# Kernel optimization log

Hardware: AMD Instinct MI355X
Metric: run time of the kernel (lower is better)

## Reference

```python
import jax, jax.numpy as jnp
import numpy as np
from jax.ops import segment_sum


def gcn_conv(x, src, dst, W, b, num_nodes):
    # PyG GCNConv: x' = D^{-1/2} (A + I) D^{-1/2} (x @ W) + b
    loops = jnp.arange(num_nodes, dtype=src.dtype)
    s = jnp.concatenate([src, loops])  # source of each edge (incl. self-loops)
    d = jnp.concatenate([dst, loops])  # destination of each edge
    ones = jnp.ones(s.shape[0], dtype=x.dtype)
    deg = segment_sum(ones, d, num_segments=num_nodes)  # in-degree incl. self-loop
    dinv = jnp.where(deg > 0, jax.lax.rsqrt(deg), 0.0)
    norm = dinv[s] * dinv[d]  # [E+N]
    h = x @ W  # [N, C_out] dense transform first (C_out <= C_in typical)
    msg = h[s] * norm[:, None]  # gather + scale  [E+N, C_out]
    out = segment_sum(msg, d, num_segments=num_nodes)  # scatter-add
    return out + b


def setup_inputs() -> dict:
    key = jax.random.key(0)
    k1, k2, k3, k4 = jax.random.split(key, 4)
    N, E = 100000, 1600000
    C_in, C_out = 64, 32
    C_hid = 2 * C_out
    x = jax.random.normal(k1, (N, C_in), dtype=jnp.float32)
    edge_index = jax.random.randint(k2, (2, E), 0, N, dtype=jnp.int64)
    # Glorot-style init for the linear weights, zero bias (PyG defaults)
    W1 = jax.random.normal(k3, (C_in, C_hid), dtype=jnp.float32) * (1.0 / np.sqrt(C_in))
    b1 = jnp.zeros((C_hid,), dtype=jnp.float32)
    W2 = jax.random.normal(k4, (C_hid, C_out), dtype=jnp.float32) * (1.0 / np.sqrt(C_hid))
    b2 = jnp.zeros((C_out,), dtype=jnp.float32)
    return {"x": x, "edge_index": edge_index, "num_nodes": N,
            "W1": W1, "b1": b1, "W2": W2, "b2": b2}


def reference(x, edge_index, num_nodes, W1, b1, W2, b2):
    src, dst = edge_index[0], edge_index[1]
    h = gcn_conv(x, src, dst, W1, b1, num_nodes)
    h = jax.nn.relu(h)
    out = gcn_conv(h, src, dst, W2, b2, num_nodes)
    return out
```

## Files before the change

kernel.cpp:

```cpp
#include <hip/hip_runtime.h>


constexpr int CAP = 8192;
constexpr int NBMAX = 512;

__device__ inline unsigned short f2bf(float f) {
    unsigned u = __float_as_uint(f);
    u += 0x7fff + ((u >> 16) & 1);
    return (unsigned short)(u >> 16);
}
__device__ inline float bflo(unsigned u) { return __uint_as_float(u << 16); }
__device__ inline float bfhi(unsigned u) { return __uint_as_float(u & 0xffff0000u); }

__global__ __launch_bounds__(256) void p1_bin(const int* __restrict__ src,
                                              const int* __restrict__ dst,
                                              int* __restrict__ bucketCursor,
                                              unsigned* __restrict__ staging, int E, int NB) {
    __shared__ int cnt[NBMAX];
    __shared__ int cur[NBMAX];
    int tid = threadIdx.x;
    for (int i = tid; i < NB; i += 256) cnt[i] = 0;
    __syncthreads();
    int e0 = blockIdx.x * 4096;
#pragma unroll
    for (int k = 0; k < 16; ++k) {
        int e = e0 + k * 256 + tid;
        if (e < E) atomicAdd(&cnt[dst[e] >> 8], 1);
    }
    __syncthreads();
    for (int i = tid; i < NB; i += 256) {
        int c = cnt[i];
        cur[i] = c ? atomicAdd(&bucketCursor[i], c) : 0;
    }
    __syncthreads();
#pragma unroll
    for (int k = 0; k < 16; ++k) {
        int e = e0 + k * 256 + tid;
        if (e < E) {
            int d = dst[e];
            int b = d >> 8;
            int slot = atomicAdd(&cur[b], 1);
            staging[(size_t)b * CAP + slot] = ((unsigned)src[e] << 8) | (unsigned)(d & 255);
        }
    }
}

__global__ __launch_bounds__(512) void scan_buckets(const int* __restrict__ bucketCursor,
                                                    int* __restrict__ bucketBase,
                                                    int* __restrict__ rp, int NB, int N, int E) {
    __shared__ int s[NBMAX];
    int tid = threadIdx.x;
    int v = (tid < NB) ? bucketCursor[tid] : 0;
    s[tid] = v;
    __syncthreads();
    for (int off = 1; off < 512; off <<= 1) {
        int t = (tid >= off) ? s[tid - off] : 0;
        __syncthreads();
        s[tid] += t;
        __syncthreads();
    }
    if (tid < NB) bucketBase[tid] = s[tid] - v;
    if (tid == 0) {
        bucketBase[NB] = E;
        rp[N] = E;
    }
}

__global__ __launch_bounds__(256) void p2_csr(const unsigned* __restrict__ staging,
                                              const int* __restrict__ bucketBase,
                                              int* __restrict__ rp, int* __restrict__ col,
                                              float* __restrict__ dinv, int N) {
    __shared__ int deg[256];
    __shared__ int scn[256];
    __shared__ int cur[256];
    int b = blockIdx.x;
    int tid = threadIdx.x;
    int base = bucketBase[b];
    int size = bucketBase[b + 1] - base;
    const unsigned* st = staging + (size_t)b * CAP;
    deg[tid] = 0;
    __syncthreads();
    for (int i = tid; i < size; i += 256) atomicAdd(&deg[st[i] & 255u], 1);
    __syncthreads();
    int g = b * 256 + tid;
    int d = deg[tid];
    if (g < N) dinv[g] = rsqrtf((float)(d + 1));
    scn[tid] = d;
    __syncthreads();
    for (int off = 1; off < 256; off <<= 1) {
        int t = (tid >= off) ? scn[tid - off] : 0;
        __syncthreads();
        scn[tid] += t;
        __syncthreads();
    }
    int excl = scn[tid] - d;
    if (g < N) rp[g] = base + excl;
    cur[tid] = excl;
    __syncthreads();
    for (int i = tid; i < size; i += 256) {
        unsigned pk = st[i];
        int pos = atomicAdd(&cur[pk & 255u], 1);
        col[base + pos] = (int)(pk >> 8);
    }
}

__global__ __launch_bounds__(256) void gemm1(const float* __restrict__ X,
                                             const float* __restrict__ W,
                                             const float* __restrict__ dinv,
                                             unsigned short* __restrict__ Hout, int N) {
    constexpr int XS = 65;
    __shared__ float Xs[128 * XS];
    __shared__ float Ws[64 * 64];
    int tid = threadIdx.x;
    int rowBase = blockIdx.x * 128;
    const float4* Wv = (const float4*)W;
    float4* Wsv = (float4*)Ws;
    for (int i = tid; i < 64 * 64 / 4; i += 256) Wsv[i] = Wv[i];
    const float4* Xv = (const float4*)X;
    for (int v = tid; v < 128 * 16; v += 256) {
        int r = v >> 4, j = v & 15;
        int gr = rowBase + r;
        float4 t = make_float4(0.f, 0.f, 0.f, 0.f);
        if (gr < N) t = Xv[(size_t)gr * 16 + j];
        int b = r * XS + j * 4;
        Xs[b] = t.x;
        Xs[b + 1] = t.y;
        Xs[b + 2] = t.z;
        Xs[b + 3] = t.w;
    }
    __syncthreads();
    int cg = tid % 8, rg = tid / 8;
    int c0 = cg * 8, r0 = rg * 4;
    float acc[4][8];
#pragma unroll
    for (int i = 0; i < 4; ++i)
#pragma unroll
        for (int j = 0; j < 8; ++j) acc[i][j] = 0.f;
#pragma unroll 8
    for (int k = 0; k < 64; ++k) {
        float4 w0 = *(const float4*)&Ws[k * 64 + c0];
        float4 w1 = *(const float4*)&Ws[k * 64 + c0 + 4];
        float xr[4];
#pragma unroll
        for (int i = 0; i < 4; ++i) xr[i] = Xs[(r0 + i) * XS + k];
#pragma unroll
        for (int i = 0; i < 4; ++i) {
            acc[i][0] = fmaf(xr[i], w0.x, acc[i][0]);
            acc[i][1] = fmaf(xr[i], w0.y, acc[i][1]);
            acc[i][2] = fmaf(xr[i], w0.z, acc[i][2]);
            acc[i][3] = fmaf(xr[i], w0.w, acc[i][3]);
            acc[i][4] = fmaf(xr[i], w1.x, acc[i][4]);
            acc[i][5] = fmaf(xr[i], w1.y, acc[i][5]);
            acc[i][6] = fmaf(xr[i], w1.z, acc[i][6]);
            acc[i][7] = fmaf(xr[i], w1.w, acc[i][7]);
        }
    }
#pragma unroll
    for (int i = 0; i < 4; ++i) {
        int row = rowBase + r0 + i;
        if (row >= N) continue;
        float dn = dinv[row];
        unsigned pk[4];
#pragma unroll
        for (int j = 0; j < 4; ++j) {
            unsigned lo = f2bf(acc[i][2 * j] * dn);
            unsigned hi = f2bf(acc[i][2 * j + 1] * dn);
            pk[j] = lo | (hi << 16);
        }
        *(uint4*)(Hout + (size_t)row * 64 + c0) = make_uint4(pk[0], pk[1], pk[2], pk[3]);
    }
}

__global__ __launch_bounds__(256) void agg1_gemm2(
    const uint4* __restrict__ hs1, const float* __restrict__ dinv, const int* __restrict__ rp,
    const int* __restrict__ col, const float* __restrict__ b1, const float* __restrict__ W2,
    unsigned short* __restrict__ h2, int N) {
    constexpr int RS = 68;
    __shared__ float rows[32 * RS];
    __shared__ float Ws2[64 * 32];
    int tid = threadIdx.x;
    const float4* W2v = (const float4*)W2;
    float4* Ws2v = (float4*)Ws2;
    for (int i = tid; i < 64 * 32 / 4; i += 256) Ws2v[i] = W2v[i];

    int r = tid >> 3, q = tid & 7;
    int node = blockIdx.x * 32 + r;
    float acc[8];
#pragma unroll
    for (int j = 0; j < 8; ++j) acc[j] = 0.f;
    float dn = 0.f;
    if (node < N) {
        dn = dinv[node];
        uint4 u = hs1[(size_t)node * 8 + q];
        acc[0] = bflo(u.x); acc[1] = bfhi(u.x);
        acc[2] = bflo(u.y); acc[3] = bfhi(u.y);
        acc[4] = bflo(u.z); acc[5] = bfhi(u.z);
        acc[6] = bflo(u.w); acc[7] = bfhi(u.w);
        int e0 = rp[node], e1 = rp[node + 1];
        int e = e0;
#define ACC8(U)                               \
    acc[0] += bflo(U.x); acc[1] += bfhi(U.x); \
    acc[2] += bflo(U.y); acc[3] += bfhi(U.y); \
    acc[4] += bflo(U.z); acc[5] += bfhi(U.z); \
    acc[6] += bflo(U.w); acc[7] += bfhi(U.w);
        for (; e + 4 <= e1; e += 4) {
            int s0 = col[e], s1 = col[e + 1], s2 = col[e + 2], s3 = col[e + 3];
            uint4 u0 = hs1[(size_t)s0 * 8 + q];
            uint4 u1 = hs1[(size_t)s1 * 8 + q];
            uint4 u2 = hs1[(size_t)s2 * 8 + q];
            uint4 u3 = hs1[(size_t)s3 * 8 + q];
            ACC8(u0) ACC8(u1) ACC8(u2) ACC8(u3)
        }
        for (; e < e1; ++e) {
            uint4 uu = hs1[(size_t)col[e] * 8 + q];
            ACC8(uu)
        }
#undef ACC8
        const float4* bv = (const float4*)b1;
        float4 bb0 = bv[q * 2], bb1 = bv[q * 2 + 1];
        acc[0] = fmaxf(fmaf(acc[0], dn, bb0.x), 0.f);
        acc[1] = fmaxf(fmaf(acc[1], dn, bb0.y), 0.f);
        acc[2] = fmaxf(fmaf(acc[2], dn, bb0.z), 0.f);
        acc[3] = fmaxf(fmaf(acc[3], dn, bb0.w), 0.f);
        acc[4] = fmaxf(fmaf(acc[4], dn, bb1.x), 0.f);
        acc[5] = fmaxf(fmaf(acc[5], dn, bb1.y), 0.f);
        acc[6] = fmaxf(fmaf(acc[6], dn, bb1.z), 0.f);
        acc[7] = fmaxf(fmaf(acc[7], dn, bb1.w), 0.f);
    }
    float* myrow = &rows[r * RS + q * 8];
    *(float4*)myrow = make_float4(acc[0], acc[1], acc[2], acc[3]);
    *(float4*)(myrow + 4) = make_float4(acc[4], acc[5], acc[6], acc[7]);
    __syncthreads();

    if (node >= N) return;
    int c0 = q * 4;
    float acc2[4] = {0.f, 0.f, 0.f, 0.f};
    const float* row = &rows[r * RS];
#pragma unroll
    for (int k4 = 0; k4 < 16; ++k4) {
        float4 xq = *(const float4*)&row[k4 * 4];
        float4 wa = *(const float4*)&Ws2[(k4 * 4 + 0) * 32 + c0];
        float4 wb = *(const float4*)&Ws2[(k4 * 4 + 1) * 32 + c0];
        float4 wc = *(const float4*)&Ws2[(k4 * 4 + 2) * 32 + c0];
        float4 wd = *(const float4*)&Ws2[(k4 * 4 + 3) * 32 + c0];
        acc2[0] = fmaf(xq.x, wa.x, acc2[0]);
        acc2[1] = fmaf(xq.x, wa.y, acc2[1]);
        acc2[2] = fmaf(xq.x, wa.z, acc2[2]);
        acc2[3] = fmaf(xq.x, wa.w, acc2[3]);
        acc2[0] = fmaf(xq.y, wb.x, acc2[0]);
        acc2[1] = fmaf(xq.y, wb.y, acc2[1]);
        acc2[2] = fmaf(xq.y, wb.z, acc2[2]);
        acc2[3] = fmaf(xq.y, wb.w, acc2[3]);
        acc2[0] = fmaf(xq.z, wc.x, acc2[0]);
        acc2[1] = fmaf(xq.z, wc.y, acc2[1]);
        acc2[2] = fmaf(xq.z, wc.z, acc2[2]);
        acc2[3] = fmaf(xq.z, wc.w, acc2[3]);
        acc2[0] = fmaf(xq.w, wd.x, acc2[0]);
        acc2[1] = fmaf(xq.w, wd.y, acc2[1]);
        acc2[2] = fmaf(xq.w, wd.z, acc2[2]);
        acc2[3] = fmaf(xq.w, wd.w, acc2[3]);
    }
    unsigned p0 = f2bf(acc2[0] * dn) | ((unsigned)f2bf(acc2[1] * dn) << 16);
    unsigned p1 = f2bf(acc2[2] * dn) | ((unsigned)f2bf(acc2[3] * dn) << 16);
    *(uint2*)(h2 + (size_t)node * 32 + c0) = make_uint2(p0, p1);
}

__global__ __launch_bounds__(256) void agg2(const uint4* __restrict__ hs2,
                                            const float* __restrict__ dinv,
                                            const int* __restrict__ rp,
                                            const int* __restrict__ col,
                                            const float* __restrict__ bias,
                                            float* __restrict__ out, int N) {
    int t = blockIdx.x * blockDim.x + threadIdx.x;
    int node = t >> 2, q = t & 3;
    if (node >= N) return;
    float acc[8];
    uint4 u = hs2[(size_t)node * 4 + q];
    acc[0] = bflo(u.x); acc[1] = bfhi(u.x);
    acc[2] = bflo(u.y); acc[3] = bfhi(u.y);
    acc[4] = bflo(u.z); acc[5] = bfhi(u.z);
    acc[6] = bflo(u.w); acc[7] = bfhi(u.w);
    int e0 = rp[node], e1 = rp[node + 1];
    int e = e0;
#define ACC8(U)                               \
    acc[0] += bflo(U.x); acc[1] += bfhi(U.x); \
    acc[2] += bflo(U.y); acc[3] += bfhi(U.y); \
    acc[4] += bflo(U.z); acc[5] += bfhi(U.z); \
    acc[6] += bflo(U.w); acc[7] += bfhi(U.w);
    for (; e + 4 <= e1; e += 4) {
        int s0 = col[e], s1 = col[e + 1], s2 = col[e + 2], s3 = col[e + 3];
        uint4 u0 = hs2[(size_t)s0 * 4 + q];
        uint4 u1 = hs2[(size_t)s1 * 4 + q];
        uint4 u2 = hs2[(size_t)s2 * 4 + q];
        uint4 u3 = hs2[(size_t)s3 * 4 + q];
        ACC8(u0) ACC8(u1) ACC8(u2) ACC8(u3)
    }
    for (; e < e1; ++e) {
        uint4 uu = hs2[(size_t)col[e] * 4 + q];
        ACC8(uu)
    }
#undef ACC8
    float dn = dinv[node];
    const float4* bv = (const float4*)bias;
    float4 b0 = bv[q * 2], b1 = bv[q * 2 + 1];
    float4 r0, r1;
    r0.x = fmaf(acc[0], dn, b0.x);
    r0.y = fmaf(acc[1], dn, b0.y);
    r0.z = fmaf(acc[2], dn, b0.z);
    r0.w = fmaf(acc[3], dn, b0.w);
    r1.x = fmaf(acc[4], dn, b1.x);
    r1.y = fmaf(acc[5], dn, b1.y);
    r1.z = fmaf(acc[6], dn, b1.z);
    r1.w = fmaf(acc[7], dn, b1.w);
    float4* ov = (float4*)(out + (size_t)node * 32 + q * 8);
    ov[0] = r0;
    ov[1] = r1;
}

extern "C" void kernel_launch(void* const* d_in, const int* in_sizes, int n_in,
                              void* d_out, int out_size, void* d_ws, size_t ws_size,
                              hipStream_t stream) {
    const float* x = (const float*)d_in[0];
    const int* ei = (const int*)d_in[1];
    const float* W1 = (const float*)d_in[3];
    const float* b1 = (const float*)d_in[4];
    const float* W2 = (const float*)d_in[5];
    const float* b2 = (const float*)d_in[6];

    constexpr int CIN = 64, CHID = 64;
    const int N = in_sizes[0] / CIN;
    const int E = in_sizes[1] / 2;
    const int* src = ei;
    const int* dst = ei + E;
    const int NB = (N + 255) >> 8;

    char* p = (char*)d_ws;
    auto carve = [&](size_t bytes) -> void* {
        void* q = (void*)p;
        p += (bytes + 255) & ~(size_t)255;
        return q;
    };
    int* bucketCursor = (int*)carve((size_t)NB * 4);
    int* bucketBase = (int*)carve((size_t)(NB + 1) * 4);
    int* rp = (int*)carve((size_t)(N + 1) * 4);
    int* col = (int*)carve((size_t)E * 4);
    float* dinv = (float*)carve((size_t)N * 4);
    unsigned* staging = (unsigned*)carve((size_t)NB * CAP * 4);
    unsigned short* h1 = (unsigned short*)carve((size_t)N * CHID * 2);
    unsigned short* h2 = (unsigned short*)staging;

    hipMemsetAsync(bucketCursor, 0, (size_t)NB * 4, stream);
    p1_bin<<<(E + 4095) / 4096, 256, 0, stream>>>(src, dst, bucketCursor, staging, E, NB);
    scan_buckets<<<1, 512, 0, stream>>>(bucketCursor, bucketBase, rp, NB, N, E);
    p2_csr<<<NB, 256, 0, stream>>>(staging, bucketBase, rp, col, dinv, N);

    gemm1<<<(N + 127) / 128, 256, 0, stream>>>(x, W1, dinv, h1, N);
    agg1_gemm2<<<(N + 31) / 32, 256, 0, stream>>>((const uint4*)h1, dinv, rp, col, b1, W2, h2, N);
    agg2<<<((size_t)N * 4 + 255) / 256, 256, 0, stream>>>((const uint4*)h2, dinv, rp, col, b2,
                                                          (float*)d_out, N);
}
```

Measured before the change: 207.6 us.

## Fold bucket scan into CSR build and add dynamic node scheduling to aggregations

Removes the single-block scan_buckets launch: each p2_csr block now redundantly prefix-sums the bucket counts in shared memory to find its own base. Both aggregation kernels now handle more nodes per block (64 and 128), and node groups take the next node from a shared-memory atomic counter. This balances uneven per-node degree inside a block. The second GEMM is remapped to four threads per node with eight outputs each and uint4 stores. The cost is extra redundant scan work per block and atomic traffic in shared memory.

```diff
diff --git a/kernel.cpp b/kernel.cpp
--- a/kernel.cpp
+++ b/kernel.cpp
@@ -45,41 +45,33 @@
     }
 }
 
-__global__ __launch_bounds__(512) void scan_buckets(const int* __restrict__ bucketCursor,
-                                                    int* __restrict__ bucketBase,
-                                                    int* __restrict__ rp, int NB, int N, int E) {
-    __shared__ int s[NBMAX];
-    int tid = threadIdx.x;
-    int v = (tid < NB) ? bucketCursor[tid] : 0;
-    s[tid] = v;
-    __syncthreads();
-    for (int off = 1; off < 512; off <<= 1) {
-        int t = (tid >= off) ? s[tid - off] : 0;
-        __syncthreads();
-        s[tid] += t;
-        __syncthreads();
-    }
-    if (tid < NB) bucketBase[tid] = s[tid] - v;
-    if (tid == 0) {
-        bucketBase[NB] = E;
-        rp[N] = E;
-    }
-}
-
 __global__ __launch_bounds__(256) void p2_csr(const unsigned* __restrict__ staging,
-                                              const int* __restrict__ bucketBase,
+                                              const int* __restrict__ bucketCursor,
                                               int* __restrict__ rp, int* __restrict__ col,
-                                              float* __restrict__ dinv, int N) {
+                                              float* __restrict__ dinv, int N, int E, int NB) {
+    __shared__ int sb[NBMAX];
     __shared__ int deg[256];
     __shared__ int scn[256];
     __shared__ int cur[256];
     int b = blockIdx.x;
     int tid = threadIdx.x;
-    int base = bucketBase[b];
-    int size = bucketBase[b + 1] - base;
+    int i1 = tid, i2 = tid + 256;
+    sb[i1] = (i1 < NB) ? bucketCursor[i1] : 0;
+    sb[i2] = (i2 < NB) ? bucketCursor[i2] : 0;
+    deg[tid] = 0;
+    __syncthreads();
+    for (int off = 1; off < NBMAX; off <<= 1) {
+        int a = (i1 >= off) ? sb[i1 - off] : 0;
+        int c = (i2 >= off) ? sb[i2 - off] : 0;
+        __syncthreads();
+        sb[i1] += a;
+        sb[i2] += c;
+        __syncthreads();
+    }
+    int base = (b == 0) ? 0 : sb[b - 1];
+    int size = sb[b] - base;
+    if (b == 0 && tid == 0) rp[N] = E;
     const unsigned* st = staging + (size_t)b * CAP;
-    deg[tid] = 0;
-    __syncthreads();
     for (int i = tid; i < size; i += 256) atomicAdd(&deg[st[i] & 255u], 1);
     __syncthreads();
     int g = b * 256 + tid;
@@ -176,93 +168,104 @@
     const int* __restrict__ col, const float* __restrict__ b1, const float* __restrict__ W2,
     unsigned short* __restrict__ h2, int N) {
     constexpr int RS = 68;
-    __shared__ float rows[32 * RS];
+    constexpr int NPB = 64;
+    __shared__ float rows[NPB * RS];
     __shared__ float Ws2[64 * 32];
+    __shared__ int ctr;
     int tid = threadIdx.x;
     const float4* W2v = (const float4*)W2;
     float4* Ws2v = (float4*)Ws2;
     for (int i = tid; i < 64 * 32 / 4; i += 256) Ws2v[i] = W2v[i];
-
-    int r = tid >> 3, q = tid & 7;
-    int node = blockIdx.x * 32 + r;
-    float acc[8];
-#pragma unroll
-    for (int j = 0; j < 8; ++j) acc[j] = 0.f;
-    float dn = 0.f;
-    if (node < N) {
-        dn = dinv[node];
-        uint4 u = hs1[(size_t)node * 8 + q];
-        acc[0] = bflo(u.x); acc[1] = bfhi(u.x);
-        acc[2] = bflo(u.y); acc[3] = bfhi(u.y);
-        acc[4] = bflo(u.z); acc[5] = bfhi(u.z);
-        acc[6] = bflo(u.w); acc[7] = bfhi(u.w);
-        int e0 = rp[node], e1 = rp[node + 1];
-        int e = e0;
+    if (tid == 0) ctr = 32;
+    __syncthreads();
+
+    int lane = tid & 63;
+    int gbase = lane & ~7;
+    int q = tid & 7;
+    int cur = tid >> 3;
+    int blockBase = blockIdx.x * NPB;
+    while (cur < NPB) {
+        int node = blockBase + cur;
+        if (node < N) {
+            float dn = dinv[node];
+            float acc[8];
+            uint4 u = hs1[(size_t)node * 8 + q];
+            acc[0] = bflo(u.x); acc[1] = bfhi(u.x);
+            acc[2] = bflo(u.y); acc[3] = bfhi(u.y);
+            acc[4] = bflo(u.z); acc[5] = bfhi(u.z);
+            acc[6] = bflo(u.w); acc[7] = bfhi(u.w);
+            int e0 = rp[node], e1 = rp[node + 1];
+            int e = e0;
 #define ACC8(U)                               \
     acc[0] += bflo(U.x); acc[1] += bfhi(U.x); \
     acc[2] += bflo(U.y); acc[3] += bfhi(U.y); \
     acc[4] += bflo(U.z); acc[5] += bfhi(U.z); \
     acc[6] += bflo(U.w); acc[7] += bfhi(U.w);
-        for (; e + 4 <= e1; e += 4) {
-            int s0 = col[e], s1 = col[e + 1], s2 = col[e + 2], s3 = col[e + 3];
-            uint4 u0 = hs1[(size_t)s0 * 8 + q];
-            uint4 u1 = hs1[(size_t)s1 * 8 + q];
-            uint4 u2 = hs1[(size_t)s2 * 8 + q];
-            uint4 u3 = hs1[(size_t)s3 * 8 + q];
-            ACC8(u0) ACC8(u1) ACC8(u2) ACC8(u3)
-        }
-        for (; e < e1; ++e) {
-            uint4 uu = hs1[(size_t)col[e] * 8 + q];
-            ACC8(uu)
-        }
+            for (; e + 4 <= e1; e += 4) {
+                int s0 = col[e], s1 = col[e + 1], s2 = col[e + 2], s3 = col[e + 3];
+                uint4 u0 = hs1[(size_t)s0 * 8 + q];
+                uint4 u1 = hs1[(size_t)s1 * 8 + q];
+                uint4 u2 = hs1[(size_t)s2 * 8 + q];
+                uint4 u3 = hs1[(size_t)s3 * 8 + q];
+                ACC8(u0) ACC8(u1) ACC8(u2) ACC8(u3)
+            }
+            for (; e < e1; ++e) {
+                uint4 uu = hs1[(size_t)col[e] * 8 + q];
+                ACC8(uu)
+            }
 #undef ACC8
-        const float4* bv = (const float4*)b1;
-        float4 bb0 = bv[q * 2], bb1 = bv[q * 2 + 1];
-        acc[0] = fmaxf(fmaf(acc[0], dn, bb0.x), 0.f);
-        acc[1] = fmaxf(fmaf(acc[1], dn, bb0.y), 0.f);
-        acc[2] = fmaxf(fmaf(acc[2], dn, bb0.z), 0.f);
-        acc[3] = fmaxf(fmaf(acc[3], dn, bb0.w), 0.f);
-        acc[4] = fmaxf(fmaf(acc[4], dn, bb1.x), 0.f);
-        acc[5] = fmaxf(fmaf(acc[5], dn, bb1.y), 0.f);
-        acc[6] = fmaxf(fmaf(acc[6], dn, bb1.z), 0.f);
-        acc[7] = fmaxf(fmaf(acc[7], dn, bb1.w), 0.f);
-    }
-    float* myrow = &rows[r * RS + q * 8];
-    *(float4*)myrow = make_float4(acc[0], acc[1], acc[2], acc[3]);
-    *(float4*)(myrow + 4) = make_float4(acc[4], acc[5], acc[6], acc[7]);
-    __syncthreads();
-
+            const float4* bv = (const float4*)b1;
+            float4 bb0 = bv[q * 2], bb1 = bv[q * 2 + 1];
+            float* myrow = &rows[cur * RS + q * 8];
+            *(float4*)myrow =
+                make_float4(fmaxf(fmaf(acc[0], dn, bb0.x), 0.f), fmaxf(fmaf(acc[1], dn, bb0.y), 0.f),
+                            fmaxf(fmaf(acc[2], dn, bb0.z), 0.f), fmaxf(fmaf(acc[3], dn, bb0.w), 0.f));
+            *(float4*)(myrow + 4) =
+                make_float4(fmaxf(fmaf(acc[4], dn, bb1.x), 0.f), fmaxf(fmaf(acc[5], dn, bb1.y), 0.f),
+                            fmaxf(fmaf(acc[6], dn, bb1.z), 0.f), fmaxf(fmaf(acc[7], dn, bb1.w), 0.f));
+        }
+        int nxt = 0;
+        if (q == 0) nxt = atomicAdd(&ctr, 1);
+        nxt = __shfl(nxt, gbase, 64);
+        cur = nxt;
+    }
+    __syncthreads();
+
+    int r = tid >> 2;
+    int c0 = (tid & 3) * 8;
+    int node = blockBase + r;
     if (node >= N) return;
-    int c0 = q * 4;
-    float acc2[4] = {0.f, 0.f, 0.f, 0.f};
+    float dn = dinv[node];
+    float acc2[8];
+#pragma unroll
+    for (int j = 0; j < 8; ++j) acc2[j] = 0.f;
     const float* row = &rows[r * RS];
 #pragma unroll
     for (int k4 = 0; k4 < 16; ++k4) {
         float4 xq = *(const float4*)&row[k4 * 4];
-        float4 wa = *(const float4*)&Ws2[(k4 * 4 + 0) * 32 + c0];
-        float4 wb = *(const float4*)&Ws2[(k4 * 4 + 1) * 32 + c0];
-        float4 wc = *(const float4*)&Ws2[(k4 * 4 + 2) * 32 + c0];
-        float4 wd = *(const float4*)&Ws2[(k4 * 4 + 3) * 32 + c0];
-        acc2[0] = fmaf(xq.x, wa.x, acc2[0]);
-        acc2[1] = fmaf(xq.x, wa.y, acc2[1]);
-        acc2[2] = fmaf(xq.x, wa.z, acc2[2]);
-        acc2[3] = fmaf(xq.x, wa.w, acc2[3]);
-        acc2[0] = fmaf(xq.y, wb.x, acc2[0]);
-        acc2[1] = fmaf(xq.y, wb.y, acc2[1]);
-        acc2[2] = fmaf(xq.y, wb.z, acc2[2]);
-        acc2[3] = fmaf(xq.y, wb.w, acc2[3]);
-        acc2[0] = fmaf(xq.z, wc.x, acc2[0]);
-        acc2[1] = fmaf(xq.z, wc.y, acc2[1]);
-        acc2[2] = fmaf(xq.z, wc.z, acc2[2]);
-        acc2[3] = fmaf(xq.z, wc.w, acc2[3]);
-        acc2[0] = fmaf(xq.w, wd.x, acc2[0]);
-        acc2[1] = fmaf(xq.w, wd.y, acc2[1]);
-        acc2[2] = fmaf(xq.w, wd.z, acc2[2]);
-        acc2[3] = fmaf(xq.w, wd.w, acc2[3]);
-    }
-    unsigned p0 = f2bf(acc2[0] * dn) | ((unsigned)f2bf(acc2[1] * dn) << 16);
-    unsigned p1 = f2bf(acc2[2] * dn) | ((unsigned)f2bf(acc2[3] * dn) << 16);
-    *(uint2*)(h2 + (size_t)node * 32 + c0) = make_uint2(p0, p1);
+#pragma unroll
+        for (int kk = 0; kk < 4; ++kk) {
+            float xv = (&xq.x)[kk];
+            float4 wa = *(const float4*)&Ws2[(k4 * 4 + kk) * 32 + c0];
+            float4 wb = *(const float4*)&Ws2[(k4 * 4 + kk) * 32 + c0 + 4];
+            acc2[0] = fmaf(xv, wa.x, acc2[0]);
+            acc2[1] = fmaf(xv, wa.y, acc2[1]);
+            acc2[2] = fmaf(xv, wa.z, acc2[2]);
+            acc2[3] = fmaf(xv, wa.w, acc2[3]);
+            acc2[4] = fmaf(xv, wb.x, acc2[4]);
+            acc2[5] = fmaf(xv, wb.y, acc2[5]);
+            acc2[6] = fmaf(xv, wb.z, acc2[6]);
+            acc2[7] = fmaf(xv, wb.w, acc2[7]);
+        }
+    }
+    unsigned pk[4];
+#pragma unroll
+    for (int j = 0; j < 4; ++j) {
+        unsigned lo = f2bf(acc2[2 * j] * dn);
+        unsigned hi = f2bf(acc2[2 * j + 1] * dn);
+        pk[j] = lo | (hi << 16);
+    }
+    *(uint4*)(h2 + (size_t)node * 32 + c0) = make_uint4(pk[0], pk[1], pk[2], pk[3]);
 }
 
 __global__ __launch_bounds__(256) void agg2(const uint4* __restrict__ hs2,
@@ -271,50 +274,59 @@
                                             const int* __restrict__ col,
                                             const float* __restrict__ bias,
                                             float* __restrict__ out, int N) {
-    int t = blockIdx.x * blockDim.x + threadIdx.x;
-    int node = t >> 2, q = t & 3;
-    if (node >= N) return;
-    float acc[8];
-    uint4 u = hs2[(size_t)node * 4 + q];
-    acc[0] = bflo(u.x); acc[1] = bfhi(u.x);
-    acc[2] = bflo(u.y); acc[3] = bfhi(u.y);
-    acc[4] = bflo(u.z); acc[5] = bfhi(u.z);
-    acc[6] = bflo(u.w); acc[7] = bfhi(u.w);
-    int e0 = rp[node], e1 = rp[node + 1];
-    int e = e0;
+    constexpr int NPB = 128;
+    __shared__ int ctr;
+    int tid = threadIdx.x;
+    if (tid == 0) ctr = 64;
+    __syncthreads();
+    int lane = tid & 63;
+    int gbase = lane & ~3;
+    int q = tid & 3;
+    int cur = tid >> 2;
+    int blockBase = blockIdx.x * NPB;
+    while (cur < NPB) {
+        int node = blockBase + cur;
+        if (node < N) {
+            float acc[8];
+            uint4 u = hs2[(size_t)node * 4 + q];
+            acc[0] = bflo(u.x); acc[1] = bfhi(u.x);
+            acc[2] = bflo(u.y); acc[3] = bfhi(u.y);
+            acc[4] = bflo(u.z); acc[5] = bfhi(u.z);
+            acc[6] = bflo(u.w); acc[7] = bfhi(u.w);
+            int e0 = rp[node], e1 = rp[node + 1];
+            int e = e0;
 #define ACC8(U)                               \
     acc[0] += bflo(U.x); acc[1] += bfhi(U.x); \
     acc[2] += bflo(U.y); acc[3] += bfhi(U.y); \
     acc[4] += bflo(U.z); acc[5] += bfhi(U.z); \
     acc[6] += bflo(U.w); acc[7] += bfhi(U.w);
-    for (; e + 4 <= e1; e += 4) {
-        int s0 = col[e], s1 = col[e + 1], s2 = col[e + 2], s3 = col[e + 3];
-        uint4 u0 = hs2[(size_t)s0 * 4 + q];
-        uint4 u1 = hs2[(size_t)s1 * 4 + q];
-        uint4 u2 = hs2[(size_t)s2 * 4 + q];
-        uint4 u3 = hs2[(size_t)s3 * 4 + q];
-        ACC8(u0) ACC8(u1) ACC8(u2) ACC8(u3)
-    }
-    for (; e < e1; ++e) {
-        uint4 uu = hs2[(size_t)col[e] * 4 + q];
-        ACC8(uu)
-    }
+            for (; e + 4 <= e1; e += 4) {
+                int s0 = col[e], s1 = col[e + 1], s2 = col[e + 2], s3 = col[e + 3];
+                uint4 u0 = hs2[(size_t)s0 * 4 + q];
+                uint4 u1 = hs2[(size_t)s1 * 4 + q];
+                uint4 u2 = hs2[(size_t)s2 * 4 + q];
+                uint4 u3 = hs2[(size_t)s3 * 4 + q];
+                ACC8(u0) ACC8(u1) ACC8(u2) ACC8(u3)
+            }
+            for (; e < e1; ++e) {
+                uint4 uu = hs2[(size_t)col[e] * 4 + q];
+                ACC8(uu)
+            }
 #undef ACC8
-    float dn = dinv[node];
-    const float4* bv = (const float4*)bias;
-    float4 b0 = bv[q * 2], b1 = bv[q * 2 + 1];
-    float4 r0, r1;
-    r0.x = fmaf(acc[0], dn, b0.x);
-    r0.y = fmaf(acc[1], dn, b0.y);
-    r0.z = fmaf(acc[2], dn, b0.z);
-    r0.w = fmaf(acc[3], dn, b0.w);
-    r1.x = fmaf(acc[4], dn, b1.x);
-    r1.y = fmaf(acc[5], dn, b1.y);
-    r1.z = fmaf(acc[6], dn, b1.z);
-    r1.w = fmaf(acc[7], dn, b1.w);
-    float4* ov = (float4*)(out + (size_t)node * 32 + q * 8);
-    ov[0] = r0;
-    ov[1] = r1;
+            float dn = dinv[node];
+            const float4* bv = (const float4*)bias;
+            float4 b0 = bv[q * 2], b1 = bv[q * 2 + 1];
+            float4* ov = (float4*)(out + (size_t)node * 32 + q * 8);
+            ov[0] = make_float4(fmaf(acc[0], dn, b0.x), fmaf(acc[1], dn, b0.y),
+                                fmaf(acc[2], dn, b0.z), fmaf(acc[3], dn, b0.w));
+            ov[1] = make_float4(fmaf(acc[4], dn, b1.x), fmaf(acc[5], dn, b1.y),
+                                fmaf(acc[6], dn, b1.z), fmaf(acc[7], dn, b1.w));
+        }
+        int nxt = 0;
+        if (q == 0) nxt = atomicAdd(&ctr, 1);
+        nxt = __shfl(nxt, gbase, 64);
+        cur = nxt;
+    }
 }
 
 extern "C" void kernel_launch(void* const* d_in, const int* in_sizes, int n_in,
@@ -341,7 +353,6 @@
         return q;
     };
     int* bucketCursor = (int*)carve((size_t)NB * 4);
-    int* bucketBase = (int*)carve((size_t)(NB + 1) * 4);
     int* rp = (int*)carve((size_t)(N + 1) * 4);
     int* col = (int*)carve((size_t)E * 4);
     float* dinv = (float*)carve((size_t)N * 4);
@@ -351,11 +362,10 @@
 
     hipMemsetAsync(bucketCursor, 0, (size_t)NB * 4, stream);
     p1_bin<<<(E + 4095) / 4096, 256, 0, stream>>>(src, dst, bucketCursor, staging, E, NB);
-    scan_buckets<<<1, 512, 0, stream>>>(bucketCursor, bucketBase, rp, NB, N, E);
-    p2_csr<<<NB, 256, 0, stream>>>(staging, bucketBase, rp, col, dinv, N);
+    p2_csr<<<NB, 256, 0, stream>>>(staging, bucketCursor, rp, col, dinv, N, E, NB);
 
     gemm1<<<(N + 127) / 128, 256, 0, stream>>>(x, W1, dinv, h1, N);
-    agg1_gemm2<<<(N + 31) / 32, 256, 0, stream>>>((const uint4*)h1, dinv, rp, col, b1, W2, h2, N);
-    agg2<<<((size_t)N * 4 + 255) / 256, 256, 0, stream>>>((const uint4*)h2, dinv, rp, col, b2,
-                                                          (float*)d_out, N);
-}
+    agg1_gemm2<<<(N + 63) / 64, 256, 0, stream>>>((const uint4*)h1, dinv, rp, col, b1, W2, h2, N);
+    agg2<<<(N + 127) / 128, 256, 0, stream>>>((const uint4*)h2, dinv, rp, col, b2, (float*)d_out,
+                                              N);
+}
```

New measurement: 220.2 us. 1.06x slower.
